# Kernel tuning notes

Hardware: AMD Instinct MI355X
Metric: run time of the kernel (lower is better)

Reference implementation:

```python
import jax, jax.numpy as jnp
import numpy as np

K = 8  # repeat(1,1,1,9) in the source forces k+1 == 9
LRELU_SLOPE = 0.01  # nn.LeakyReLU default negative slope


def knn_idx(x, k):
    """x: [B, C, N] -> indices of k nearest points [B, N, k] (largest neg sq dist)."""
    xx = jnp.sum(x * x, axis=1)                       # [B, N]
    inner = jnp.einsum('bcn,bcm->bnm', x, x)          # [B, N, N]
    neg_sq_dist = 2.0 * inner - xx[:, :, None] - xx[:, None, :]
    return jax.lax.top_k(neg_sq_dist, k)[1]           # [B, N, k]


def gather_neighbors(feat, idx):
    """feat: [B, C, N], idx: [B, N, k] -> [B, C, N, k] (grouping_operation)."""
    return jax.vmap(lambda f, i: f[:, i])(feat, idx)


def setup_inputs() -> dict:
    key = jax.random.key(0)
    k1, k2, k3 = jax.random.split(key, 3)
    B, C, N = 8, 128, 4096
    points = jax.random.normal(k1, (B, C, N), dtype=jnp.float32)
    # xavier_uniform-ish init for W [C, 1]
    limit = 1.414 * np.sqrt(6.0 / (C + 1))
    W = jax.random.uniform(k2, (C, 1), dtype=jnp.float32, minval=-limit, maxval=limit)
    conv2_w = jax.random.normal(k3, (C, C), dtype=jnp.float32) * 0.05
    return {"points": points, "W": W, "conv2_w": conv2_w}


def reference(points, W, conv2_w):
    # points: [B, C, N]
    shortcut = points
    # knn on raw (detached) features -> integer indices, no grad path
    idx = knn_idx(jax.lax.stop_gradient(points), K)            # [B, N, K]
    features = jax.nn.leaky_relu(points, LRELU_SLOPE)          # [B, C, N]
    grouped_points = gather_neighbors(features, idx)           # [B, C, N, K]
    center_points = features[:, :, :, None]                    # [B, C, N, 1]
    feats = jnp.concatenate([grouped_points, center_points], axis=3)  # [B, C, N, K+1]
    feats = jnp.transpose(feats, (0, 2, 3, 1))                 # [B, N, K+1, C]
    att = jnp.einsum('bnkc,co->bnko', feats, W)                # [B, N, K+1, 1]
    att = jax.nn.softmax(att, axis=2)                          # softmax over K+1 neighbors
    # repeat(1,1,1,9) then matmul: out[b,n,i,c] = att[b,n,i] * sum_j feats[b,n,j,c]
    # followed by mean over i -> mean_i(att) * sum_j(feats)
    s = jnp.sum(feats, axis=2)                                 # [B, N, C]
    out = jnp.mean(att, axis=2) * s                            # [B, N, C]
    out = jnp.transpose(out, (0, 2, 1)) + shortcut             # [B, C, N]
    # 1x1 conv residual branch on grouped neighbor features
    grouped_points_nn = jnp.einsum('oc,bcnk->bonk', conv2_w, grouped_points)  # [B, C, N, K]
    return (out, grouped_points_nn)
```

## Files before the change

kernel.cpp:

```cpp
#include <hip/hip_runtime.h>
#include <cstdint>
#include <cstddef>

#define BB_ 8
#define CC_ 128
#define NN_ 4096
#define KK_ 8

#define XX_OFF  0
#define IDX_OFF 32768
#define G_OFF   294912

__device__ __forceinline__ float lrelu(float v) { return v >= 0.f ? v : 0.01f * v; }

template <int S>
__device__ __forceinline__ void insert_tieup(float (&v)[S], int (&ix)[S], float d, int m) {
  if (d < v[S - 1]) return;
  bool bs[S];
#pragma unroll
  for (int s = 0; s < S; ++s) bs[s] = (v[s] > d);
#pragma unroll
  for (int s = S - 1; s >= 1; --s) {
    v[s]  = bs[s] ? v[s]  : (bs[s - 1] ? d : v[s - 1]);
    ix[s] = bs[s] ? ix[s] : (bs[s - 1] ? m : ix[s - 1]);
  }
  if (!bs[0]) { v[0] = d; ix[0] = m; }
}

template <int S>
__device__ __forceinline__ void insert_ti_desc(float (&v)[S], int (&ix)[S], float d, int m) {
  bool stay = (v[S - 1] > d) || (v[S - 1] == d && ix[S - 1] > m);
  if (stay) return;
  bool bs[S];
#pragma unroll
  for (int s = 0; s < S; ++s) bs[s] = (v[s] > d) || (v[s] == d && ix[s] > m);
#pragma unroll
  for (int s = S - 1; s >= 1; --s) {
    v[s]  = bs[s] ? v[s]  : (bs[s - 1] ? d : v[s - 1]);
    ix[s] = bs[s] ? ix[s] : (bs[s - 1] ? m : ix[s - 1]);
  }
  if (!bs[0]) { v[0] = d; ix[0] = m; }
}

__global__ void k_xx(const float* __restrict__ x, float* __restrict__ out1f) {
  int t = blockIdx.x * 256 + threadIdx.x;
  int b = t >> 12, n = t & (NN_ - 1);
  const float* p = x + ((size_t)b * CC_) * NN_ + n;
  float acc = 0.f;
  {
#pragma clang fp contract(off)
#pragma unroll
    for (int c = 0; c < CC_; ++c) {
      float v = p[(size_t)c * NN_];
      float v2 = v * v;
      acc = acc + v2;
    }
  }
  out1f[XX_OFF + t] = acc;
}

__device__ __forceinline__ void fma16(float (&acc)[4][4], const float4 (&a)[4],
                                      const float4 (&b)[4]) {
#pragma unroll
  for (int i = 0; i < 4; ++i)
#pragma unroll
    for (int j = 0; j < 4; ++j) {
      acc[i][j] = fmaf(a[i].x, b[j].x, acc[i][j]);
      acc[i][j] = fmaf(a[i].y, b[j].y, acc[i][j]);
      acc[i][j] = fmaf(a[i].z, b[j].z, acc[i][j]);
      acc[i][j] = fmaf(a[i].w, b[j].w, acc[i][j]);
    }
}

__global__ __launch_bounds__(256, 3) void k_knn(const float* __restrict__ x,
                                                float* __restrict__ out1f) {
  __shared__ __align__(16) union S {
    struct {
      float As[64 * 132];
      float Bs[64 * 68];
      float xxm[64];
    } a;
    struct { float v[4 * 64 * 9]; int i[4 * 64 * 9]; } mg;
  } s;

  const float* xxz = out1f + XX_OFF;
  int* idxz = (int*)(out1f + IDX_OFF);

  const int blk = blockIdx.x;
  const int b = blk >> 6;
  const int n0 = (blk & 63) << 6;
  const float* xb = x + ((size_t)b * CC_) * NN_;
  const int t = threadIdx.x;
  const int tr = t & 15, tc = t >> 4;
  const int r64 = t & 63, wv = t >> 6;

  {
#pragma unroll
    for (int q = 0; q < 8; ++q) {
      int g = wv + 4 * q;
      float4 tmp;
      tmp.x = xb[(size_t)(4 * g + 0) * NN_ + n0 + r64];
      tmp.y = xb[(size_t)(4 * g + 1) * NN_ + n0 + r64];
      tmp.z = xb[(size_t)(4 * g + 2) * NN_ + n0 + r64];
      tmp.w = xb[(size_t)(4 * g + 3) * NN_ + n0 + r64];
      *reinterpret_cast<float4*>(&s.a.As[r64 * 132 + 4 * g]) = tmp;
    }
  }

  float xr[4];
#pragma unroll
  for (int i = 0; i < 4; ++i) xr[i] = xxz[(b << 12) + n0 + tr + 16 * i];

  float lv[4][8]; int li[4][8];
#pragma unroll
  for (int i = 0; i < 4; ++i)
#pragma unroll
    for (int q = 0; q < 8; ++q) { lv[i][q] = -INFINITY; li[i][q] = 0x7FFFFFFF; }

  const float4* As4 = reinterpret_cast<const float4*>(s.a.As);
  const float4* Bs4 = reinterpret_cast<const float4*>(s.a.Bs);
  int rowA[4], rowB[4];
#pragma unroll
  for (int i = 0; i < 4; ++i) rowA[i] = (tr + 16 * i) * 33;
#pragma unroll
  for (int j = 0; j < 4; ++j) rowB[j] = (tc * 4 + j) * 17;

  for (int m0 = 0; m0 < NN_; m0 += 64) {
    float acc[4][4] = {};
#pragma unroll
    for (int p = 0; p < 2; ++p) {
      __syncthreads();
      {
#pragma unroll
        for (int q = 0; q < 4; ++q) {
          int gl = wv + 4 * q;
          int c0 = 64 * p + 4 * gl;
          float4 tmp;
          tmp.x = xb[(size_t)(c0 + 0) * NN_ + m0 + r64];
          tmp.y = xb[(size_t)(c0 + 1) * NN_ + m0 + r64];
          tmp.z = xb[(size_t)(c0 + 2) * NN_ + m0 + r64];
          tmp.w = xb[(size_t)(c0 + 3) * NN_ + m0 + r64];
          *reinterpret_cast<float4*>(&s.a.Bs[r64 * 68 + 4 * gl]) = tmp;
        }
        if (p == 0 && t < 64) s.a.xxm[t] = xxz[(b << 12) + m0 + t];
      }
      __syncthreads();

#pragma unroll 2
      for (int gl = 0; gl < 16; ++gl) {
        float4 av[4], bv[4];
#pragma unroll
        for (int i = 0; i < 4; ++i) av[i] = As4[rowA[i] + 16 * p + gl];
#pragma unroll
        for (int j = 0; j < 4; ++j) bv[j] = Bs4[rowB[j] + gl];
        fma16(acc, av, bv);
      }
    }

#pragma unroll
    for (int j = 0; j < 4; ++j) {
      float xm = s.a.xxm[tc * 4 + j];
      int m = m0 + tc * 4 + j;
#pragma unroll
      for (int i = 0; i < 4; ++i) {
        float d = (2.0f * acc[i][j] - xr[i]) - xm;
        insert_tieup<8>(lv[i], li[i], d, m);
      }
    }
  }

  __syncthreads();
#pragma unroll
  for (int mk = 16; mk <= 32; mk <<= 1) {
#pragma unroll
    for (int i = 0; i < 4; ++i) {
      float pv[8]; int pi[8];
#pragma unroll
      for (int q = 0; q < 8; ++q) {
        pv[q] = __shfl_xor(lv[i][q], mk, 64);
        pi[q] = __shfl_xor(li[i][q], mk, 64);
      }
#pragma unroll
      for (int q = 0; q < 8; ++q) insert_ti_desc<8>(lv[i], li[i], pv[q], pi[q]);
    }
  }
  if ((t & 63) < 16) {
#pragma unroll
    for (int i = 0; i < 4; ++i) {
      int base = wv * 576 + (tr + 16 * i) * 9;
#pragma unroll
      for (int q = 0; q < 8; ++q) {
        s.mg.v[base + q] = lv[i][q];
        s.mg.i[base + q] = li[i][q];
      }
    }
  }
  __syncthreads();
  if (t < 64) {
    float bvv[8]; int bii[8];
#pragma unroll
    for (int q = 0; q < 8; ++q) { bvv[q] = s.mg.v[t * 9 + q]; bii[q] = s.mg.i[t * 9 + q]; }
#pragma unroll
    for (int w = 1; w < 4; ++w) {
      int base = w * 576 + t * 9;
#pragma unroll
      for (int q = 0; q < 8; ++q) insert_ti_desc<8>(bvv, bii, s.mg.v[base + q], s.mg.i[base + q]);
    }
    int* op = idxz + (b << 15) + ((n0 + t) << 3);
#pragma unroll
    for (int q = 0; q < KK_; ++q) op[q] = bii[q];
  }
}

__global__ __launch_bounds__(256) void k_gemm(const float* __restrict__ x,
                                              const float* __restrict__ w2,
                                              float* __restrict__ out1f) {
  __shared__ __align__(16) float Ws[64][68];
  __shared__ __align__(16) float Fs[64][68];
  int bb = blockIdx.x >> 7;
  int r = blockIdx.x & 127;
  int o0 = (r >> 6) << 6;
  int m0 = (r & 63) << 6;
  const float* xb = x + ((size_t)bb * CC_) * NN_;
  float* gb = out1f + G_OFF + ((size_t)bb * CC_) * NN_;
  int t = threadIdx.x;
  int tm = t & 15, to = t >> 4;

  float acc[4][4] = {};
  for (int cc = 0; cc < CC_; cc += 64) {
    __syncthreads();
    {
      int cl = t & 63, q0 = t >> 6;
      for (int oo = q0; oo < 64; oo += 4) Ws[oo][cl] = w2[(o0 + oo) * CC_ + cc + cl];
      for (int c2 = q0; c2 < 64; c2 += 4) Fs[cl][c2] = lrelu(xb[(size_t)(cc + c2) * NN_ + m0 + cl]);
    }
    __syncthreads();
#pragma unroll 8
    for (int cq = 0; cq < 64; cq += 4) {
      float4 aw[4], bf[4];
#pragma unroll
      for (int i = 0; i < 4; ++i) aw[i] = *reinterpret_cast<const float4*>(&Ws[to + 16 * i][cq]);
#pragma unroll
      for (int j = 0; j < 4; ++j) bf[j] = *reinterpret_cast<const float4*>(&Fs[tm + 16 * j][cq]);
#pragma unroll
      for (int i = 0; i < 4; ++i)
#pragma unroll
        for (int j = 0; j < 4; ++j) {
          acc[i][j] = fmaf(aw[i].x, bf[j].x, acc[i][j]);
          acc[i][j] = fmaf(aw[i].y, bf[j].y, acc[i][j]);
          acc[i][j] = fmaf(aw[i].z, bf[j].z, acc[i][j]);
          acc[i][j] = fmaf(aw[i].w, bf[j].w, acc[i][j]);
        }
    }
  }
#pragma unroll
  for (int i = 0; i < 4; ++i)
#pragma unroll
    for (int j = 0; j < 4; ++j)
      gb[((size_t)(o0 + to + 16 * i)) * NN_ + m0 + tm + 16 * j] = acc[i][j];
}

__global__ void k_out0(const float* __restrict__ x, const float* __restrict__ out1f,
                       float* __restrict__ out) {
  __shared__ int idxL[512];
  int b = blockIdx.x >> 6, nt = blockIdx.x & 63;
  int n0 = nt << 6;
  int t = threadIdx.x;
  const int* ib = (const int*)(out1f + IDX_OFF) + (b << 15) + (n0 << 3);
  idxL[t] = ib[t];
  idxL[t + 256] = ib[t + 256];
  __syncthreads();
  int nl = t & 63, c0 = t >> 6;
  for (int c = c0; c < CC_; c += 4) {
    const float* row = x + ((size_t)b * CC_ + c) * NN_;
    float self = row[n0 + nl];
    float s = 0.f;
#pragma unroll
    for (int k = 0; k < KK_; ++k) s += lrelu(row[idxL[(nl << 3) + k]]);
    s += lrelu(self);
    out[((size_t)b * CC_ + c) * NN_ + n0 + nl] = fmaf(s, 1.0f / 9.0f, self);
  }
}

__global__ void k_gatherA(float* __restrict__ out1f) {
  int bc = 137 + blockIdx.x;
  int b = bc >> 7;
  const int* idxz = (const int*)(out1f + IDX_OFF) + (b << 15);
  const float* gs = out1f + G_OFF + (size_t)bc * (size_t)NN_;
  float* op = out1f + (size_t)bc * 32768;
  for (int e = threadIdx.x; e < 32768; e += 256) {
    op[e] = gs[idxz[e]];
  }
}

__global__ __launch_bounds__(256) void k_gatherB(const float* __restrict__ x,
                                                 const float* __restrict__ w2,
                                                 float* __restrict__ out1f) {
  __shared__ int idxL[512];
  __shared__ float xcols[8][128];
  int T = blockIdx.x;
  int t = threadIdx.x;
  const int* idxz = (const int*)(out1f + IDX_OFF);
  idxL[t]       = idxz[0 * 32768 + ((T * 32) << 3) + t];
  idxL[t + 256] = idxz[1 * 32768 + ((T * 32) << 3) + t];
  __syncthreads();

  for (int it = 0; it < 64; ++it) {
    int colbase = it * 8;
    {
      int cg = t >> 5, lane = t & 31;
      int col = colbase + cg;
      int bsel = col >> 8;
      int m = idxL[col];
      const float* xb = x + ((size_t)bsel * CC_) * NN_;
#pragma unroll
      for (int q = 0; q < 4; ++q) {
        int c = lane + 32 * q;
        xcols[cg][c] = lrelu(xb[(size_t)c * NN_ + m]);
      }
    }
    __syncthreads();
    {
      int cg = t >> 5, c0 = t & 31;
      int col = colbase + cg;
      int bsel = col >> 8;
      int rk = col & 255;
      int n = T * 32 + (rk >> 3);
      int k = rk & 7;
      int hmax = (bsel == 0) ? 4 : 1;
      for (int h = 0; h < hmax; ++h) {
        int c = c0 + 32 * h;
        const float* wr = w2 + c * CC_;
        float acc = 0.f;
#pragma unroll 8
        for (int cc = 0; cc < CC_; ++cc) acc = fmaf(wr[cc], xcols[cg][cc], acc);
        if (bsel == 0 || c <= 8) {
          out1f[(size_t)(bsel * CC_ + c) * 32768 + (n << 3) + k] = acc;
        }
      }
    }
    __syncthreads();
  }
}

extern "C" void kernel_launch(void* const* d_in, const int* in_sizes, int n_in,
                              void* d_out, int out_size, void* d_ws, size_t ws_size,
                              hipStream_t stream) {
  const float* x  = (const float*)d_in[0];
  const float* w2 = (const float*)d_in[2];

  float* out0  = (float*)d_out;
  float* out1f = out0 + (size_t)BB_ * CC_ * NN_;
  (void)d_ws; (void)ws_size;

  k_xx     <<<(BB_ * NN_) / 256,  256, 0, stream>>>(x, out1f);
  k_knn    <<<BB_ * (NN_ / 64),   256, 0, stream>>>(x, out1f);
  k_gemm   <<<BB_ * 128,          256, 0, stream>>>(x, w2, out1f);
  k_out0   <<<BB_ * 64,           256, 0, stream>>>(x, out1f, out0);
  k_gatherA<<<1024 - 137,         256, 0, stream>>>(out1f);
  k_gatherB<<<128,                256, 0, stream>>>(x, w2, out1f);
}
```

Measured before the change: 2.522 ms.

## Split KNN candidate range across two blocks and read pre-transposed features directly

Adds a transpose kernel that writes x as [B,N,C] into the output scratch area. The KNN kernel then reads B-tile operands straight from global/L2 as float4 rows instead of staging them through shared memory with syncs. Each query tile is now split into two blocks covering half the candidate range, which doubles the grid to fill more CUs. A new merge kernel combines the two partial top-8 lists. The changes add an extra transpose pass, partial-result traffic and two more kernel launches, and they rely on L2 hits for the uncached B reads.

```diff
diff --git a/kernel.cpp b/kernel.cpp
--- a/kernel.cpp
+++ b/kernel.cpp
@@ -10,6 +10,9 @@
 #define XX_OFF  0
 #define IDX_OFF 32768
 #define G_OFF   294912
+#define PV_OFF  6815744
+#define PI_OFF  7340032
+#define XT_OFF  16777216
 
 __device__ __forceinline__ float lrelu(float v) { return v >= 0.f ? v : 0.01f * v; }
 
@@ -40,6 +43,25 @@
     ix[s] = bs[s] ? ix[s] : (bs[s - 1] ? m : ix[s - 1]);
   }
   if (!bs[0]) { v[0] = d; ix[0] = m; }
+}
+
+__global__ __launch_bounds__(256) void k_xt(const float* __restrict__ x,
+                                            float* __restrict__ out1f) {
+  __shared__ float Ls[64][132];
+  int b = blockIdx.x >> 6, mt = blockIdx.x & 63;
+  int m0 = mt << 6;
+  int t = threadIdx.x;
+  const float* xb = x + ((size_t)b * CC_) * NN_;
+  {
+    int ml = t & 63, c0 = t >> 6;
+    for (int c = c0; c < CC_; c += 4) Ls[ml][c] = xb[(size_t)c * NN_ + m0 + ml];
+  }
+  __syncthreads();
+  float* xTb = out1f + XT_OFF + (size_t)(b << 12) * CC_;
+  {
+    int cl = t & 127, r0 = t >> 7;
+    for (int r = r0; r < 64; r += 2) xTb[(size_t)(m0 + r) * CC_ + cl] = Ls[r][cl];
+  }
 }
 
 __global__ void k_xx(const float* __restrict__ x, float* __restrict__ out1f) {
@@ -75,37 +97,38 @@
 __global__ __launch_bounds__(256, 3) void k_knn(const float* __restrict__ x,
                                                 float* __restrict__ out1f) {
   __shared__ __align__(16) union S {
-    struct {
-      float As[64 * 132];
-      float Bs[64 * 68];
-      float xxm[64];
-    } a;
+    float As[64 * 132];
     struct { float v[4 * 64 * 9]; int i[4 * 64 * 9]; } mg;
   } s;
 
   const float* xxz = out1f + XX_OFF;
-  int* idxz = (int*)(out1f + IDX_OFF);
+  const float* xT  = out1f + XT_OFF;
+  float* pvz = out1f + PV_OFF;
+  int*   piz = (int*)(out1f + PI_OFF);
 
   const int blk = blockIdx.x;
-  const int b = blk >> 6;
-  const int n0 = (blk & 63) << 6;
-  const float* xb = x + ((size_t)b * CC_) * NN_;
+  const int b  = blk >> 7;
+  const int nt = (blk >> 1) & 63;
+  const int h  = blk & 1;
+  const int n0 = nt << 6;
+  const int m_base = h << 11;
   const int t = threadIdx.x;
   const int tr = t & 15, tc = t >> 4;
-  const int r64 = t & 63, wv = t >> 6;
+  const int wv = t >> 6;
+
+  const float* xTb = xT + (size_t)(b << 12) * CC_;
 
   {
+    int r = t & 63, q0 = t >> 6;
+    const float4* src = reinterpret_cast<const float4*>(xTb + (size_t)(n0 + r) * CC_);
+    float4* dst = reinterpret_cast<float4*>(s.As) + r * 33;
 #pragma unroll
     for (int q = 0; q < 8; ++q) {
-      int g = wv + 4 * q;
-      float4 tmp;
-      tmp.x = xb[(size_t)(4 * g + 0) * NN_ + n0 + r64];
-      tmp.y = xb[(size_t)(4 * g + 1) * NN_ + n0 + r64];
-      tmp.z = xb[(size_t)(4 * g + 2) * NN_ + n0 + r64];
-      tmp.w = xb[(size_t)(4 * g + 3) * NN_ + n0 + r64];
-      *reinterpret_cast<float4*>(&s.a.As[r64 * 132 + 4 * g]) = tmp;
-    }
-  }
+      int g = q0 + 4 * q;
+      dst[g] = src[g];
+    }
+  }
+  __syncthreads();
 
   float xr[4];
 #pragma unroll
@@ -117,53 +140,33 @@
 #pragma unroll
     for (int q = 0; q < 8; ++q) { lv[i][q] = -INFINITY; li[i][q] = 0x7FFFFFFF; }
 
-  const float4* As4 = reinterpret_cast<const float4*>(s.a.As);
-  const float4* Bs4 = reinterpret_cast<const float4*>(s.a.Bs);
-  int rowA[4], rowB[4];
+  const float4* As4 = reinterpret_cast<const float4*>(s.As);
+  int rowA[4];
 #pragma unroll
   for (int i = 0; i < 4; ++i) rowA[i] = (tr + 16 * i) * 33;
-#pragma unroll
-  for (int j = 0; j < 4; ++j) rowB[j] = (tc * 4 + j) * 17;
-
-  for (int m0 = 0; m0 < NN_; m0 += 64) {
+
+  for (int m0c = 0; m0c < 2048; m0c += 64) {
+    const int m0 = m_base + m0c;
+    const float4* b0p = reinterpret_cast<const float4*>(xTb + (size_t)(m0 + tc * 4) * CC_);
     float acc[4][4] = {};
-#pragma unroll
-    for (int p = 0; p < 2; ++p) {
-      __syncthreads();
-      {
-#pragma unroll
-        for (int q = 0; q < 4; ++q) {
-          int gl = wv + 4 * q;
-          int c0 = 64 * p + 4 * gl;
-          float4 tmp;
-          tmp.x = xb[(size_t)(c0 + 0) * NN_ + m0 + r64];
-          tmp.y = xb[(size_t)(c0 + 1) * NN_ + m0 + r64];
-          tmp.z = xb[(size_t)(c0 + 2) * NN_ + m0 + r64];
-          tmp.w = xb[(size_t)(c0 + 3) * NN_ + m0 + r64];
-          *reinterpret_cast<float4*>(&s.a.Bs[r64 * 68 + 4 * gl]) = tmp;
-        }
-        if (p == 0 && t < 64) s.a.xxm[t] = xxz[(b << 12) + m0 + t];
-      }
-      __syncthreads();
-
-#pragma unroll 2
-      for (int gl = 0; gl < 16; ++gl) {
-        float4 av[4], bv[4];
-#pragma unroll
-        for (int i = 0; i < 4; ++i) av[i] = As4[rowA[i] + 16 * p + gl];
-#pragma unroll
-        for (int j = 0; j < 4; ++j) bv[j] = Bs4[rowB[j] + gl];
-        fma16(acc, av, bv);
-      }
-    }
-
+#pragma unroll 4
+    for (int g = 0; g < 32; ++g) {
+      float4 av[4], bv[4];
+#pragma unroll
+      for (int i = 0; i < 4; ++i) av[i] = As4[rowA[i] + g];
+#pragma unroll
+      for (int j = 0; j < 4; ++j) bv[j] = b0p[j * 32 + g];
+      fma16(acc, av, bv);
+    }
+
+    float4 xmv = *reinterpret_cast<const float4*>(xxz + (b << 12) + m0 + tc * 4);
+    float xma[4] = {xmv.x, xmv.y, xmv.z, xmv.w};
 #pragma unroll
     for (int j = 0; j < 4; ++j) {
-      float xm = s.a.xxm[tc * 4 + j];
       int m = m0 + tc * 4 + j;
 #pragma unroll
       for (int i = 0; i < 4; ++i) {
-        float d = (2.0f * acc[i][j] - xr[i]) - xm;
+        float d = (2.0f * acc[i][j] - xr[i]) - xma[j];
         insert_tieup<8>(lv[i], li[i], d, m);
       }
     }
@@ -206,10 +209,28 @@
 #pragma unroll
       for (int q = 0; q < 8; ++q) insert_ti_desc<8>(bvv, bii, s.mg.v[base + q], s.mg.i[base + q]);
     }
-    int* op = idxz + (b << 15) + ((n0 + t) << 3);
-#pragma unroll
-    for (int q = 0; q < KK_; ++q) op[q] = bii[q];
-  }
+    size_t rowg = (size_t)(b << 12) + n0 + t;
+    float* pvp = pvz + (rowg * 2 + h) * 8;
+    int*   pip = piz + (rowg * 2 + h) * 8;
+#pragma unroll
+    for (int q = 0; q < KK_; ++q) { pvp[q] = bvv[q]; pip[q] = bii[q]; }
+  }
+}
+
+__global__ void k_merge(float* __restrict__ out1f) {
+  int row = blockIdx.x * 256 + threadIdx.x;
+  const float* pvz = out1f + PV_OFF;
+  const int*   piz = (const int*)(out1f + PI_OFF);
+  int* idxz = (int*)(out1f + IDX_OFF);
+  const float* p0 = pvz + (size_t)row * 16;
+  const int*   i0 = piz + (size_t)row * 16;
+  float v[8]; int ix[8];
+#pragma unroll
+  for (int q = 0; q < 8; ++q) { v[q] = p0[q]; ix[q] = i0[q]; }
+#pragma unroll
+  for (int q = 0; q < 8; ++q) insert_ti_desc<8>(v, ix, p0[8 + q], i0[8 + q]);
+#pragma unroll
+  for (int q = 0; q < KK_; ++q) idxz[(size_t)row * 8 + q] = ix[q];
 }
 
 __global__ __launch_bounds__(256) void k_gemm(const float* __restrict__ x,
@@ -353,8 +374,10 @@
   float* out1f = out0 + (size_t)BB_ * CC_ * NN_;
   (void)d_ws; (void)ws_size;
 
+  k_xt     <<<BB_ * 64,           256, 0, stream>>>(x, out1f);
   k_xx     <<<(BB_ * NN_) / 256,  256, 0, stream>>>(x, out1f);
-  k_knn    <<<BB_ * (NN_ / 64),   256, 0, stream>>>(x, out1f);
+  k_knn    <<<BB_ * 128,          256, 0, stream>>>(x, out1f);
+  k_merge  <<<128,                256, 0, stream>>>(out1f);
   k_gemm   <<<BB_ * 128,          256, 0, stream>>>(x, w2, out1f);
   k_out0   <<<BB_ * 64,           256, 0, stream>>>(x, out1f, out0);
   k_gatherA<<<1024 - 137,         256, 0, stream>>>(out1f);
```

Measured after the change: 2.753 ms. 9.1% more time.

## Split KNN candidate range into two halves with separate top-k merge kernel

Applied to the files above, without the earlier changes.

The KNN kernel now splits the candidate dimension into two halves, doubling the grid from 512 to 1024 blocks. Each block writes partial top-8 values and indices to scratch space in the output buffer. A new merge kernel combines the two partial lists into the final indices. This adds parallelism for the 256-CU GPU, where 512 blocks underfill the device, at the cost of an extra launch and scratch traffic.

```diff
diff --git a/kernel.cpp b/kernel.cpp
--- a/kernel.cpp
+++ b/kernel.cpp
@@ -10,6 +10,8 @@
 #define XX_OFF  0
 #define IDX_OFF 32768
 #define G_OFF   294912
+#define PV_OFF  6815744
+#define PI_OFF  7340032
 
 __device__ __forceinline__ float lrelu(float v) { return v >= 0.f ? v : 0.01f * v; }
 
@@ -84,11 +86,15 @@
   } s;
 
   const float* xxz = out1f + XX_OFF;
-  int* idxz = (int*)(out1f + IDX_OFF);
+  float* pvz = out1f + PV_OFF;
+  int*   piz = (int*)(out1f + PI_OFF);
 
   const int blk = blockIdx.x;
-  const int b = blk >> 6;
-  const int n0 = (blk & 63) << 6;
+  const int b  = blk >> 7;
+  const int nt = (blk >> 1) & 63;
+  const int h  = blk & 1;
+  const int n0 = nt << 6;
+  const int m_base = h << 11;
   const float* xb = x + ((size_t)b * CC_) * NN_;
   const int t = threadIdx.x;
   const int tr = t & 15, tc = t >> 4;
@@ -125,7 +131,8 @@
 #pragma unroll
   for (int j = 0; j < 4; ++j) rowB[j] = (tc * 4 + j) * 17;
 
-  for (int m0 = 0; m0 < NN_; m0 += 64) {
+  for (int m0c = 0; m0c < 2048; m0c += 64) {
+    const int m0 = m_base + m0c;
     float acc[4][4] = {};
 #pragma unroll
     for (int p = 0; p < 2; ++p) {
@@ -206,10 +213,28 @@
 #pragma unroll
       for (int q = 0; q < 8; ++q) insert_ti_desc<8>(bvv, bii, s.mg.v[base + q], s.mg.i[base + q]);
     }
-    int* op = idxz + (b << 15) + ((n0 + t) << 3);
-#pragma unroll
-    for (int q = 0; q < KK_; ++q) op[q] = bii[q];
-  }
+    size_t rowg = (size_t)(b << 12) + n0 + t;
+    float* pvp = pvz + (rowg * 2 + h) * 8;
+    int*   pip = piz + (rowg * 2 + h) * 8;
+#pragma unroll
+    for (int q = 0; q < KK_; ++q) { pvp[q] = bvv[q]; pip[q] = bii[q]; }
+  }
+}
+
+__global__ void k_merge(float* __restrict__ out1f) {
+  int row = blockIdx.x * 256 + threadIdx.x;
+  const float* pvz = out1f + PV_OFF;
+  const int*   piz = (const int*)(out1f + PI_OFF);
+  int* idxz = (int*)(out1f + IDX_OFF);
+  const float* p0 = pvz + (size_t)row * 16;
+  const int*   i0 = piz + (size_t)row * 16;
+  float v[8]; int ix[8];
+#pragma unroll
+  for (int q = 0; q < 8; ++q) { v[q] = p0[q]; ix[q] = i0[q]; }
+#pragma unroll
+  for (int q = 0; q < 8; ++q) insert_ti_desc<8>(v, ix, p0[8 + q], i0[8 + q]);
+#pragma unroll
+  for (int q = 0; q < KK_; ++q) idxz[(size_t)row * 8 + q] = ix[q];
 }
 
 __global__ __launch_bounds__(256) void k_gemm(const float* __restrict__ x,
@@ -354,7 +379,8 @@
   (void)d_ws; (void)ws_size;
 
   k_xx     <<<(BB_ * NN_) / 256,  256, 0, stream>>>(x, out1f);
-  k_knn    <<<BB_ * (NN_ / 64),   256, 0, stream>>>(x, out1f);
+  k_knn    <<<BB_ * 128,          256, 0, stream>>>(x, out1f);
+  k_merge  <<<128,                256, 0, stream>>>(out1f);
   k_gemm   <<<BB_ * 128,          256, 0, stream>>>(x, w2, out1f);
   k_out0   <<<BB_ * 64,           256, 0, stream>>>(x, out1f, out0);
   k_gatherA<<<1024 - 137,         256, 0, stream>>>(out1f);
```

Result: no change. 2.473 ms (-2.0%).
